# Kernel optimization log

Hardware: AMD Instinct MI355X
Metric: run time of the kernel (lower is better)

Reference implementation:

```python
import jax, jax.numpy as jnp
import numpy as np

N, E, F, G, C, L = 20000, 320000, 75, 64, 10, 5
EPS = 1e-5


def setup_inputs():
    key = jax.random.key(0)
    ks = jax.random.split(key, 16)
    x = jax.random.normal(ks[0], (N, 6), jnp.float32)
    edge_index = jax.random.randint(ks[1], (2, E), 0, N, dtype=jnp.int32)
    batch = jnp.sort(jax.random.randint(ks[2], (N,), 0, G, dtype=jnp.int32))
    gcn_w = jax.random.normal(ks[3], (6, F), jnp.float32) / np.sqrt(6.0)
    gcn_b = jnp.zeros((F,), jnp.float32)
    pre_w = jax.random.normal(ks[4], (L, 2 * F, F), jnp.float32) / np.sqrt(2.0 * F)
    pre_b = jnp.zeros((L, F), jnp.float32)
    post_w = jax.random.normal(ks[5], (L, 13 * F, F), jnp.float32) / np.sqrt(13.0 * F)
    post_b = jnp.zeros((L, F), jnp.float32)
    lin_w = jax.random.normal(ks[6], (L, F, F), jnp.float32) / np.sqrt(1.0 * F)
    lin_b = jnp.zeros((L, F), jnp.float32)
    bn_g = jnp.ones((L, F), jnp.float32)
    bn_b = jnp.zeros((L, F), jnp.float32)
    w1 = jax.random.normal(ks[7], (F, 50), jnp.float32) / np.sqrt(1.0 * F)
    b1 = jnp.zeros((50,), jnp.float32)
    w2 = jax.random.normal(ks[8], (50, 25), jnp.float32) / np.sqrt(50.0)
    b2 = jnp.zeros((25,), jnp.float32)
    w3 = jax.random.normal(ks[9], (25, C), jnp.float32) / np.sqrt(25.0)
    b3 = jnp.zeros((C,), jnp.float32)
    return dict(x=x, edge_index=edge_index, batch=batch, gcn_w=gcn_w, gcn_b=gcn_b,
                pre_w=pre_w, pre_b=pre_b, post_w=post_w, post_b=post_b,
                lin_w=lin_w, lin_b=lin_b, bn_g=bn_g, bn_b=bn_b,
                w1=w1, b1=b1, w2=w2, b2=b2, w3=w3, b3=b3)


def reference(x, edge_index, batch, gcn_w, gcn_b, pre_w, pre_b, post_w, post_b,
              lin_w, lin_b, bn_g, bn_b, w1, b1, w2, b2, w3, b3):
    row, col = edge_index[0], edge_index[1]  # messages flow row (j) -> col (i)
    ones_e = jnp.ones((E,), jnp.float32)

    # ---- GCNConv(6, 75) with self-loops and symmetric normalization ----
    xw = x @ gcn_w                                   # [N, F]
    deg = jax.ops.segment_sum(ones_e, col, N) + 1.0  # in-degree + self-loop
    dinv = 1.0 / jnp.sqrt(deg)
    norm_e = (dinv[row] * dinv[col])[:, None]        # [E, 1]
    h = jax.ops.segment_sum(norm_e * xw[row], col, N) + (dinv * dinv)[:, None] * xw + gcn_b

    # ---- degree-based scalers (shared by all PNA layers) ----
    cnt = jax.ops.segment_sum(ones_e, col, N)        # in-degree per node
    avg_log = jnp.mean(jnp.log(cnt + 1.0))           # avg_deg['log'] from this graph's degree histogram
    d = jnp.maximum(cnt, 1.0)
    amp = (jnp.log(d + 1.0) / avg_log)[:, None]      # amplification
    att = (avg_log / jnp.log(d + 1.0))[:, None]      # attenuation
    cnt_c = jnp.maximum(cnt, 1.0)[:, None]
    has_nb = (cnt > 0)[:, None]

    for l in range(L):
        # pre-MLP on [x_i, x_j] per edge
        m = jnp.concatenate([h[col], h[row]], axis=-1) @ pre_w[l] + pre_b[l]  # [E, F]
        s = jax.ops.segment_sum(m, col, N)
        mean = s / cnt_c
        mean_sq = jax.ops.segment_sum(m * m, col, N) / cnt_c
        std = jnp.sqrt(jax.nn.relu(mean_sq - mean * mean) + EPS)
        mn = jnp.where(has_nb, jax.ops.segment_min(m, col, N), 0.0)
        mx = jnp.where(has_nb, jax.ops.segment_max(m, col, N), 0.0)
        agg = jnp.concatenate([mean, mn, mx, std], axis=-1)          # [N, 4F]
        scaled = jnp.concatenate([agg, agg * amp, agg * att], -1)    # [N, 12F]
        o = jnp.concatenate([h, scaled], axis=-1) @ post_w[l] + post_b[l]  # post-MLP
        o = o @ lin_w[l] + lin_b[l]                                  # final lin
        mu = o.mean(axis=0)
        var = o.var(axis=0)
        o = (o - mu) / jnp.sqrt(var + EPS) * bn_g[l] + bn_b[l]       # BatchNorm (batch stats)
        h = jax.nn.relu(o)

    # ---- global_add_pool + MLP (dropout = identity in eval) ----
    g = jax.ops.segment_sum(h, batch, G)
    g = jax.nn.relu(g @ w1 + b1)
    g = jax.nn.relu(g @ w2 + b2)
    return g @ w3 + b3  # [G, C]
```

## Files before the change

### kernel.cpp

```cpp
#include <hip/hip_runtime.h>
#include <hip/hip_bf16.h>

#define NN 20000
#define EE 320000
#define FF 75
#define GG 64
#define LL 5
#define EPS 1e-5f

#define KUV 96
#define NUV 160
#define KPOST 384
#define NPOST 240
#define KLIN 96

typedef short bf16x8 __attribute__((ext_vector_type(8)));
typedef float f32x4 __attribute__((ext_vector_type(4)));

__device__ inline void gAtomicAdd(float* p, float v) { unsafeAtomicAdd(p, v); }

__device__ inline ushort f2bs(float x) {
    __hip_bfloat16 b = __float2bfloat16(x);
    return *(ushort*)&b;
}

__device__ inline float bs2f(ushort u) {
    unsigned int x = ((unsigned int)u) << 16;
    return __uint_as_float(x);
}


__global__ void count_kernel(const int* __restrict__ col, int* __restrict__ cnt, int E) {
    int e = blockIdx.x * blockDim.x + threadIdx.x;
    if (e < E) atomicAdd(&cnt[col[e]], 1);
}

__global__ void partial_kernel(const int* __restrict__ cnt, int* __restrict__ bsum, int N) {
    __shared__ int sh[256];
    int tid = threadIdx.x;
    int i = blockIdx.x * 256 + tid;
    sh[tid] = (i < N) ? cnt[i] : 0;
    __syncthreads();
    for (int s = 128; s > 0; s >>= 1) {
        if (tid < s) sh[tid] += sh[tid + s];
        __syncthreads();
    }
    if (tid == 0) bsum[blockIdx.x] = sh[0];
}

__global__ void scanb_kernel(const int* __restrict__ bsum, int* __restrict__ bbase,
                             int* __restrict__ offs, int NB) {
    __shared__ int sh[128];
    int tid = threadIdx.x;
    int v = (tid < NB) ? bsum[tid] : 0;
    sh[tid] = v;
    __syncthreads();
    for (int d = 1; d < 128; d <<= 1) {
        int t = (tid >= d) ? sh[tid - d] : 0;
        __syncthreads();
        sh[tid] += t;
        __syncthreads();
    }
    if (tid < NB) bbase[tid] = sh[tid] - v;
    if (tid == 0) offs[NN] = EE;
}

__global__ void offs_kernel(const int* __restrict__ cnt, const int* __restrict__ bbase,
                            int* __restrict__ offs, int* __restrict__ cursor, int N) {
    __shared__ int sh[256];
    int tid = threadIdx.x;
    int i = blockIdx.x * 256 + tid;
    int v = (i < N) ? cnt[i] : 0;
    sh[tid] = v;
    __syncthreads();
    for (int d = 1; d < 256; d <<= 1) {
        int t = (tid >= d) ? sh[tid - d] : 0;
        __syncthreads();
        sh[tid] += t;
        __syncthreads();
    }
    int excl = sh[tid] - v + bbase[blockIdx.x];
    if (i < N) { offs[i] = excl; cursor[i] = excl; }
}

__global__ void fill_kernel(const int* __restrict__ row, const int* __restrict__ col,
                            int* __restrict__ cursor, int* __restrict__ csr, int E) {
    int e = blockIdx.x * blockDim.x + threadIdx.x;
    if (e < E) {
        int c = col[e];
        int pos = atomicAdd(&cursor[c], 1);
        csr[pos] = row[e];
    }
}


__global__ void dinv_kernel(const int* __restrict__ cnt, float* __restrict__ dinv,
                            float* __restrict__ scal, int N) {
    __shared__ float red[256];
    int i = blockIdx.x * 256 + threadIdx.x;
    float lg = 0.f;
    if (i < N) {
        float c = (float)cnt[i];
        dinv[i] = 1.f / sqrtf(c + 1.f);
        lg = logf(c + 1.f);
    }
    red[threadIdx.x] = lg;
    __syncthreads();
    for (int s = 128; s > 0; s >>= 1) {
        if (threadIdx.x < s) red[threadIdx.x] += red[threadIdx.x + s];
        __syncthreads();
    }
    if (threadIdx.x == 0) gAtomicAdd(&scal[0], red[0]);
}


__global__ void xs_kernel(const float* __restrict__ x, const float* __restrict__ gw,
                          const float* __restrict__ dinv, ushort* __restrict__ xs, int N) {
    int idx = blockIdx.x * 256 + threadIdx.x;
    if (idx >= N * 80) return;
    int n = idx / 80, t = idx % 80;
    float v = 0.f;
    if (t < FF) {
        float acc = 0.f;
#pragma unroll
        for (int k = 0; k < 6; k++) acc += x[n * 6 + k] * gw[k * FF + t];
        v = dinv[n] * acc;
    }
    xs[idx] = f2bs(v);
}

__global__ __launch_bounds__(64) void gcn_kernel(
    const ushort* __restrict__ xs, const float* __restrict__ dinv,
    const int* __restrict__ offs, const int* __restrict__ csr,
    const float* __restrict__ gcn_b, const int* __restrict__ cnt,
    const float* __restrict__ scal, float* __restrict__ o2,
    float* __restrict__ amp, float* __restrict__ att, int N) {
    int i = blockIdx.x;
    int lane = threadIdx.x;
    int s0 = offs[i], s1 = offs[i + 1];
    if (lane < 40) {
        float a0 = 0.f, a1 = 0.f;
        int k = s0;
        for (; k + 1 < s1; k += 2) {
            int r0 = csr[k], r1 = csr[k + 1];
            ushort2 v0 = *(const ushort2*)(xs + (size_t)r0 * 80 + 2 * lane);
            ushort2 v1 = *(const ushort2*)(xs + (size_t)r1 * 80 + 2 * lane);
            a0 += bs2f(v0.x) + bs2f(v1.x);
            a1 += bs2f(v0.y) + bs2f(v1.y);
        }
        if (k < s1) {
            int r0 = csr[k];
            ushort2 v0 = *(const ushort2*)(xs + (size_t)r0 * 80 + 2 * lane);
            a0 += bs2f(v0.x);
            a1 += bs2f(v0.y);
        }
        ushort2 vs = *(const ushort2*)(xs + (size_t)i * 80 + 2 * lane);
        a0 += bs2f(vs.x);
        a1 += bs2f(vs.y);
        float di = dinv[i];
        int t0 = 2 * lane, t1 = 2 * lane + 1;
        if (t0 < FF) o2[(size_t)i * 80 + t0] = di * a0 + gcn_b[t0];
        if (t1 < FF) o2[(size_t)i * 80 + t1] = di * a1 + gcn_b[t1];
    } else if (lane == 63) {
        float al = scal[0] / (float)N;
        float d = fmaxf((float)cnt[i], 1.f);
        float lg = logf(d + 1.f);
        amp[i] = lg / al;
        att[i] = al / lg;
    }
}


#define S_UV (LL * NUV * KUV)
#define S_POST (LL * NPOST * KPOST)
#define S_LIN (LL * 80 * KLIN)

__global__ void prep_bt_kernel(const float* __restrict__ pre_w, const float* __restrict__ pre_b,
                               const float* __restrict__ post_w, const float* __restrict__ lin_w,
                               ushort* __restrict__ BTuv, ushort* __restrict__ BTpost,
                               ushort* __restrict__ BTlin) {
    int idx = blockIdx.x * 256 + threadIdx.x;
    if (idx < S_UV) {
        int l = idx / (NUV * KUV);
        int r = idx % (NUV * KUV);
        int c = r / KUV, k = r % KUV;
        float v = 0.f;
        if (k < FF) {
            if (c < FF) v = pre_w[((size_t)l * 150 + k) * FF + c];
            else if (c >= 80 && c < 80 + FF) v = pre_w[((size_t)l * 150 + FF + k) * FF + (c - 80)];
        } else if (k == FF && c < FF) {
            v = pre_b[l * FF + c];
        }
        BTuv[idx] = f2bs(v);
    } else if (idx < S_UV + S_POST) {
        int j = idx - S_UV;
        int l = j / (NPOST * KPOST);
        int r = j % (NPOST * KPOST);
        int c = r / KPOST, k = r % KPOST;
        float v = 0.f;
        if (k < FF) {
            if (c < FF) v = post_w[((size_t)l * 975 + k) * FF + c];
        } else if (k < 375) {
            if (c < FF) v = post_w[((size_t)l * 975 + k) * FF + c];
            else if (c >= 80 && c < 80 + FF) v = post_w[((size_t)l * 975 + k + 300) * FF + (c - 80)];
            else if (c >= 160 && c < 160 + FF) v = post_w[((size_t)l * 975 + k + 600) * FF + (c - 160)];
        }
        BTpost[j] = f2bs(v);
    } else if (idx < S_UV + S_POST + S_LIN) {
        int j = idx - S_UV - S_POST;
        int l = j / (80 * KLIN);
        int r = j % (80 * KLIN);
        int c = r / KLIN, k = r % KLIN;
        float v = (c < FF && k < FF) ? lin_w[((size_t)l * FF + k) * FF + c] : 0.f;
        BTlin[j] = f2bs(v);
    }
}


__global__ __launch_bounds__(64) void uv_bn_kernel(
    const float* __restrict__ o2, const float* __restrict__ slots,
    const float* __restrict__ bg, const float* __restrict__ bb, int apply_bn,
    const ushort* __restrict__ BT, float* __restrict__ U, ushort* __restrict__ Vb,
    ushort* __restrict__ hagg) {
    __shared__ float ssL[160];
    int lane = threadIdx.x;
    int col16 = lane & 15, quad = lane >> 4;
    int n = blockIdx.x * 16 + col16;
    const float* orow = o2 + (size_t)n * 80;
    const ushort* bbase = BT + (size_t)col16 * KUV + quad * 8;

    if (apply_bn) {
        for (int c = lane; c < 80; c += 64) {
            if (c < FF) {
                float su = 0.f, sq = 0.f;
#pragma unroll 8
                for (int s = 0; s < 32; s++) {
                    su += slots[s * 160 + c];
                    sq += slots[s * 160 + 80 + c];
                }
                float mu = su * (1.f / (float)NN);
                float var = sq * (1.f / (float)NN) - mu * mu;
                float sc = bg[c] * rsqrtf(var + EPS);
                ssL[c] = sc;
                ssL[80 + c] = bb[c] - mu * sc;
            } else {
                ssL[c] = 0.f;
                ssL[80 + c] = 0.f;
            }
        }
        __syncthreads();
    }

    f32x4 acc[10];
#pragma unroll
    for (int i = 0; i < 10; i++) acc[i] = (f32x4){0.f, 0.f, 0.f, 0.f};

#pragma unroll
    for (int kt = 0; kt < 3; kt++) {
        int kb = kt * 32 + quad * 8;
        bf16x8 af;
        if (kb < 80) {
            float4 v0 = *(const float4*)(orow + kb);
            float4 v1 = *(const float4*)(orow + kb + 4);
            float vv[8] = {v0.x, v0.y, v0.z, v0.w, v1.x, v1.y, v1.z, v1.w};
#pragma unroll
            for (int j = 0; j < 8; j++) {
                int k = kb + j;
                float v = vv[j];
                if (apply_bn) v = fmaxf(v * ssL[k] + ssL[80 + k], 0.f);
                ushort b = (k < FF) ? f2bs(v) : (k == FF ? (ushort)0x3F80 : (ushort)0);
                af[j] = (short)b;
            }
            if (kb < FF) {
                *(bf16x8*)(hagg + (size_t)n * KPOST + kb) = af;
            }
        } else {
            af = (bf16x8){0, 0, 0, 0, 0, 0, 0, 0};
        }
#pragma unroll
        for (int nt = 0; nt < 10; nt++) {
            bf16x8 bfr = *(const bf16x8*)(bbase + nt * (16 * KUV) + kt * 32);
            acc[nt] = __builtin_amdgcn_mfma_f32_16x16x32_bf16(af, bfr, acc[nt], 0, 0, 0);
        }
    }
    int n0 = blockIdx.x * 16;
#pragma unroll
    for (int nt = 0; nt < 10; nt++) {
        int col = nt * 16 + col16;
#pragma unroll
        for (int r = 0; r < 4; r++) {
            int nn = n0 + quad * 4 + r;
            if (col < FF) U[(size_t)nn * 80 + col] = acc[nt][r];
            else if (col >= 80 && col < 80 + FF) Vb[(size_t)nn * 80 + (col - 80)] = f2bs(acc[nt][r]);
        }
    }
}


__global__ __launch_bounds__(64) void post_lin_kernel(
    const ushort* __restrict__ A, const ushort* __restrict__ BT,
    const ushort* __restrict__ BL, const float* __restrict__ amp,
    const float* __restrict__ att, float* __restrict__ o2,
    float* __restrict__ slots) {
    __shared__ __align__(16) ushort olds[16 * 104];
    int lane = threadIdx.x;
    int col16 = lane & 15, quad = lane >> 4;
    int n0 = blockIdx.x * 16;
    const ushort* arow = A + (size_t)(n0 + col16) * KPOST + quad * 8;
    const ushort* bbase = BT + (size_t)col16 * KPOST + quad * 8;

    f32x4 acc[15];
#pragma unroll
    for (int i = 0; i < 15; i++) acc[i] = (f32x4){0.f, 0.f, 0.f, 0.f};

#pragma unroll 2
    for (int kt = 0; kt < 12; kt++) {
        bf16x8 af = *(const bf16x8*)(arow + kt * 32);
#pragma unroll
        for (int nt = 0; nt < 15; nt++) {
            bf16x8 bfr = *(const bf16x8*)(bbase + nt * (16 * KPOST) + kt * 32);
            acc[nt] = __builtin_amdgcn_mfma_f32_16x16x32_bf16(af, bfr, acc[nt], 0, 0, 0);
        }
    }
    float ampv[4], attv[4];
#pragma unroll
    for (int r = 0; r < 4; r++) {
        int n = n0 + quad * 4 + r;
        ampv[r] = amp[n];
        attv[r] = att[n];
    }
#pragma unroll
    for (int g = 0; g < 5; g++) {
        int col = g * 16 + col16;
#pragma unroll
        for (int r = 0; r < 4; r++) {
            float ov = acc[g][r] + ampv[r] * acc[g + 5][r] + attv[r] * acc[g + 10][r];
            olds[(quad * 4 + r) * 104 + col] = (col < FF) ? f2bs(ov) : (ushort)0;
        }
    }
    *(ushort4*)(olds + (lane >> 2) * 104 + 80 + (lane & 3) * 4) = (ushort4){0, 0, 0, 0};
    __syncthreads();

    f32x4 acc2[5];
#pragma unroll
    for (int i = 0; i < 5; i++) acc2[i] = (f32x4){0.f, 0.f, 0.f, 0.f};
    const ushort* blbase = BL + (size_t)col16 * KLIN + quad * 8;
#pragma unroll
    for (int kt = 0; kt < 3; kt++) {
        bf16x8 af = *(const bf16x8*)(olds + col16 * 104 + kt * 32 + quad * 8);
#pragma unroll
        for (int nt = 0; nt < 5; nt++) {
            bf16x8 bfr = *(const bf16x8*)(blbase + nt * (16 * KLIN) + kt * 32);
            acc2[nt] = __builtin_amdgcn_mfma_f32_16x16x32_bf16(af, bfr, acc2[nt], 0, 0, 0);
        }
    }
    float* slot = slots + (blockIdx.x & 31) * 160;
#pragma unroll
    for (int nt = 0; nt < 5; nt++) {
        int col = nt * 16 + col16;
        float s = 0.f, q = 0.f;
#pragma unroll
        for (int r = 0; r < 4; r++) {
            int n = n0 + quad * 4 + r;
            float v = acc2[nt][r];
            if (col < FF) {
                o2[(size_t)n * 80 + col] = v;
                s += v;
                q += v * v;
            }
        }
        s += __shfl_xor(s, 16); s += __shfl_xor(s, 32);
        q += __shfl_xor(q, 16); q += __shfl_xor(q, 32);
        if (lane < 16 && col < FF) {
            gAtomicAdd(&slot[col], s);
            gAtomicAdd(&slot[80 + col], q);
        }
    }
}


__global__ __launch_bounds__(64) void edge_agg_kernel(
    const float* __restrict__ U, const ushort* __restrict__ V,
    const int* __restrict__ offs, const int* __restrict__ csr,
    const int* __restrict__ cnt, ushort* __restrict__ hagg) {
    int i = blockIdx.x;
    int lane = threadIdx.x;
    int s0 = offs[i], s1 = offs[i + 1];
    if (lane < 40) {
        float2 uiv = *(const float2*)(U + (size_t)i * 80 + 2 * lane);
        float ui0 = uiv.x, ui1 = uiv.y;
        float sa0 = 0.f, sq0 = 0.f, mn0 = 1e30f, mx0 = -1e30f;
        float sa1 = 0.f, sq1 = 0.f, mn1 = 1e30f, mx1 = -1e30f;
        int k = s0;
        for (; k + 1 < s1; k += 2) {
            int r0 = csr[k], r1 = csr[k + 1];
            ushort2 v0 = *(const ushort2*)(V + (size_t)r0 * 80 + 2 * lane);
            ushort2 v1 = *(const ushort2*)(V + (size_t)r1 * 80 + 2 * lane);
            float a0 = ui0 + bs2f(v0.x), b0 = ui0 + bs2f(v1.x);
            float a1 = ui1 + bs2f(v0.y), b1 = ui1 + bs2f(v1.y);
            sa0 += a0 + b0; sq0 += a0 * a0 + b0 * b0;
            mn0 = fminf(mn0, fminf(a0, b0)); mx0 = fmaxf(mx0, fmaxf(a0, b0));
            sa1 += a1 + b1; sq1 += a1 * a1 + b1 * b1;
            mn1 = fminf(mn1, fminf(a1, b1)); mx1 = fmaxf(mx1, fmaxf(a1, b1));
        }
        if (k < s1) {
            int r0 = csr[k];
            ushort2 v0 = *(const ushort2*)(V + (size_t)r0 * 80 + 2 * lane);
            float a0 = ui0 + bs2f(v0.x);
            float a1 = ui1 + bs2f(v0.y);
            sa0 += a0; sq0 += a0 * a0; mn0 = fminf(mn0, a0); mx0 = fmaxf(mx0, a0);
            sa1 += a1; sq1 += a1 * a1; mn1 = fminf(mn1, a1); mx1 = fmaxf(mx1, a1);
        }
        int c = cnt[i];
        float cc = fmaxf((float)c, 1.f);
        ushort* a = hagg + (size_t)i * KPOST + FF;
        int t0 = 2 * lane, t1 = 2 * lane + 1;
        {
            float mean = sa0 / cc;
            float stdv = sqrtf(fmaxf(sq0 / cc - mean * mean, 0.f) + EPS);
            if (c == 0) { mn0 = 0.f; mx0 = 0.f; }
            if (t0 < FF) {
                a[t0] = f2bs(mean);
                a[FF + t0] = f2bs(mn0);
                a[2 * FF + t0] = f2bs(mx0);
                a[3 * FF + t0] = f2bs(stdv);
            }
        }
        {
            float mean = sa1 / cc;
            float stdv = sqrtf(fmaxf(sq1 / cc - mean * mean, 0.f) + EPS);
            if (c == 0) { mn1 = 0.f; mx1 = 0.f; }
            if (t1 < FF) {
                a[t1] = f2bs(mean);
                a[FF + t1] = f2bs(mn1);
                a[2 * FF + t1] = f2bs(mx1);
                a[3 * FF + t1] = f2bs(stdv);
            }
        }
    } else if (lane >= 48 && lane < 57) {
        hagg[(size_t)i * KPOST + 375 + (lane - 48)] = 0;
    }
}


__global__ void pool_kernel(const float* __restrict__ o2, const float* __restrict__ slots,
                            const float* __restrict__ bg, const float* __restrict__ bb,
                            const int* __restrict__ batch, float* __restrict__ g, int N) {
    __shared__ float acc[GG * FF];
    __shared__ float ssL[160];
    int tid = threadIdx.x;
    int n0 = blockIdx.x * 64;
    int n1 = min(n0 + 64, N);
    if (n0 >= N) return;
    for (int c = tid; c < 80; c += 256) {
        if (c < FF) {
            float su = 0.f, sq = 0.f;
#pragma unroll 8
            for (int s = 0; s < 32; s++) {
                su += slots[s * 160 + c];
                sq += slots[s * 160 + 80 + c];
            }
            float mu = su * (1.f / (float)NN);
            float var = sq * (1.f / (float)NN) - mu * mu;
            float sc = bg[c] * rsqrtf(var + EPS);
            ssL[c] = sc;
            ssL[80 + c] = bb[c] - mu * sc;
        } else {
            ssL[c] = 0.f;
            ssL[80 + c] = 0.f;
        }
    }
    int g0 = batch[n0];
    int g1 = batch[n1 - 1];
    int range = g1 - g0 + 1;
    for (int i = tid; i < range * FF; i += 256) acc[i] = 0.f;
    __syncthreads();
    int rows = n1 - n0;
    for (int idx = tid; idx < rows * FF; idx += 256) {
        int r = idx / FF, c = idx % FF;
        int n = n0 + r;
        float val = fmaxf(o2[(size_t)n * 80 + c] * ssL[c] + ssL[80 + c], 0.f);
        gAtomicAdd(&acc[(batch[n] - g0) * FF + c], val);
    }
    __syncthreads();
    for (int i = tid; i < range * FF; i += 256) gAtomicAdd(&g[g0 * FF + i], acc[i]);
}

__global__ void mlp_kernel(const float* __restrict__ g,
                           const float* __restrict__ w1, const float* __restrict__ b1,
                           const float* __restrict__ w2, const float* __restrict__ b2,
                           const float* __restrict__ w3, const float* __restrict__ b3,
                           float* __restrict__ out) {
    __shared__ float gr[FF], h1[50], h2[25];
    int gi = blockIdx.x, t = threadIdx.x;
    for (int j = t; j < FF; j += 64) gr[j] = g[gi * FF + j];
    __syncthreads();
    if (t < 50) {
        float a = b1[t];
        for (int k = 0; k < FF; k++) a += gr[k] * w1[k * 50 + t];
        h1[t] = fmaxf(a, 0.f);
    }
    __syncthreads();
    if (t < 25) {
        float a = b2[t];
        for (int k = 0; k < 50; k++) a += h1[k] * w2[k * 25 + t];
        h2[t] = fmaxf(a, 0.f);
    }
    __syncthreads();
    if (t < 10) {
        float a = b3[t];
        for (int k = 0; k < 25; k++) a += h2[k] * w3[k * 10 + t];
        out[gi * 10 + t] = a;
    }
}


extern "C" void kernel_launch(void* const* d_in, const int* in_sizes, int n_in,
                              void* d_out, int out_size, void* d_ws, size_t ws_size,
                              hipStream_t stream) {
    const float* x = (const float*)d_in[0];
    const int* ei = (const int*)d_in[1];
    const int* batch = (const int*)d_in[2];
    const float* gcn_w = (const float*)d_in[3];
    const float* gcn_b = (const float*)d_in[4];
    const float* pre_w = (const float*)d_in[5];
    const float* pre_b = (const float*)d_in[6];
    const float* post_w = (const float*)d_in[7];
    const float* lin_w = (const float*)d_in[9];
    const float* bn_g = (const float*)d_in[11];
    const float* bn_b = (const float*)d_in[12];
    const float* w1 = (const float*)d_in[13];
    const float* b1 = (const float*)d_in[14];
    const float* w2 = (const float*)d_in[15];
    const float* b2 = (const float*)d_in[16];
    const float* w3 = (const float*)d_in[17];
    const float* b3 = (const float*)d_in[18];
    float* out = (float*)d_out;

    const int* row = ei;
    const int* col = ei + EE;

    char* ws = (char*)d_ws;
    size_t off = 0;
    auto alloc = [&](size_t bytes) {
        char* p = ws + off;
        off += (bytes + 255) & ~(size_t)255;
        return p;
    };
    int* cnt = (int*)alloc(NN * 4);
    int* offs = (int*)alloc((NN + 1) * 4);
    int* cursor = (int*)alloc(NN * 4);
    int* csr = (int*)alloc(EE * 4);
    int* bsum = (int*)alloc(128 * 4);
    int* bbase = (int*)alloc(128 * 4);
    float* dinv = (float*)alloc(NN * 4);
    float* amp = (float*)alloc(NN * 4);
    float* att = (float*)alloc(NN * 4);
    float* scal = (float*)alloc((1 + LL * 32 * 160) * 4);
    float* slotbase = scal + 1;
    float* o2 = (float*)alloc((size_t)NN * 80 * 4);
    float* ubuf = (float*)alloc((size_t)NN * 80 * 4);
    ushort* vbuf = (ushort*)alloc((size_t)NN * 80 * 2);
    ushort* hagg = (ushort*)alloc((size_t)NN * KPOST * 2);
    ushort* BTuv = (ushort*)alloc((size_t)S_UV * 2);
    ushort* BTpost = (ushort*)alloc((size_t)S_POST * 2);
    ushort* BTlin = (ushort*)alloc((size_t)S_LIN * 2);
    float* gbuf = (float*)alloc(GG * FF * 4);

    hipMemsetAsync(cnt, 0, NN * 4, stream);
    hipMemsetAsync(scal, 0, (1 + LL * 32 * 160) * 4, stream);
    hipMemsetAsync(gbuf, 0, GG * FF * 4, stream);

    const int B = 256;
    const int NB = (NN + 255) / 256;
    count_kernel<<<(EE + B - 1) / B, B, 0, stream>>>(col, cnt, EE);
    dinv_kernel<<<NB, B, 0, stream>>>(cnt, dinv, scal, NN);
    partial_kernel<<<NB, B, 0, stream>>>(cnt, bsum, NN);
    scanb_kernel<<<1, 128, 0, stream>>>(bsum, bbase, offs, NB);
    offs_kernel<<<NB, B, 0, stream>>>(cnt, bbase, offs, cursor, NN);
    fill_kernel<<<(EE + B - 1) / B, B, 0, stream>>>(row, col, cursor, csr, EE);
    xs_kernel<<<(NN * 80 + B - 1) / B, B, 0, stream>>>(x, gcn_w, dinv, vbuf, NN);
    gcn_kernel<<<NN, 64, 0, stream>>>(vbuf, dinv, offs, csr, gcn_b, cnt, scal,
                                      o2, amp, att, NN);
    {
        int tot = S_UV + S_POST + S_LIN;
        prep_bt_kernel<<<(tot + B - 1) / B, B, 0, stream>>>(pre_w, pre_b, post_w, lin_w,
                                                            BTuv, BTpost, BTlin);
    }

    const int GS = NN / 16;
    for (int l = 0; l < LL; l++) {
        float* slots_prev = slotbase + (l - 1) * 32 * 160;
        float* slots = slotbase + l * 32 * 160;
        int lp = (l > 0) ? (l - 1) : 0;

        uv_bn_kernel<<<GS, 64, 0, stream>>>(o2, (l == 0) ? slotbase : slots_prev,
                                            bn_g + lp * FF, bn_b + lp * FF, (l > 0) ? 1 : 0,
                                            BTuv + (size_t)l * NUV * KUV, ubuf, vbuf, hagg);
        edge_agg_kernel<<<NN, 64, 0, stream>>>(ubuf, vbuf, offs, csr, cnt, hagg);
        post_lin_kernel<<<GS, 64, 0, stream>>>(hagg, BTpost + (size_t)l * NPOST * KPOST,
                                               BTlin + (size_t)l * 80 * KLIN, amp, att,
                                               o2, slots);
    }

    pool_kernel<<<(NN + 63) / 64, 256, 0, stream>>>(o2, slotbase + (LL - 1) * 32 * 160,
                                                    bn_g + (LL - 1) * FF, bn_b + (LL - 1) * FF,
                                                    batch, gbuf, NN);
    mlp_kernel<<<GG, 64, 0, stream>>>(gbuf, w1, b1, w2, b2, w3, b3, out);
}
```

Baseline: 509.8 us.

## Fuse edge aggregation into post/lin GEMM kernel via shared-memory staging

Merges the per-node edge aggregation kernel into the post-MLP/final-linear kernel. Each 256-thread block builds its 16-row aggregated bf16 input tile in LDS (recomputing the BN+ReLU'd h from o2) instead of writing and rereading a global hagg buffer. The GEMM N-tiles are split across four waves, with wave 0 taking a fifth tile. Separately, the dinv and partial-sum setup kernels are merged into one launch. This removes a large global round trip and per-layer launches, but aggregation now runs with only 16 nodes per block, which may cut latency hiding for the gather, and wave 0 does extra work.

```diff
diff --git a/kernel.cpp b/kernel.cpp
--- a/kernel.cpp
+++ b/kernel.cpp
@@ -13,6 +13,7 @@
 #define KPOST 384
 #define NPOST 240
 #define KLIN 96
+#define ASTR 392
 
 typedef short bf16x8 __attribute__((ext_vector_type(8)));
 typedef float f32x4 __attribute__((ext_vector_type(4)));
@@ -35,17 +36,31 @@
     if (e < E) atomicAdd(&cnt[col[e]], 1);
 }
 
-__global__ void partial_kernel(const int* __restrict__ cnt, int* __restrict__ bsum, int N) {
-    __shared__ int sh[256];
+__global__ void dinv_partial_kernel(const int* __restrict__ cnt, float* __restrict__ dinv,
+                                    float* __restrict__ scal, int* __restrict__ bsum, int N) {
+    __shared__ float red[256];
+    __shared__ int redi[256];
     int tid = threadIdx.x;
     int i = blockIdx.x * 256 + tid;
-    sh[tid] = (i < N) ? cnt[i] : 0;
+    float lg = 0.f;
+    int cv = 0;
+    if (i < N) {
+        cv = cnt[i];
+        float c = (float)cv;
+        dinv[i] = 1.f / sqrtf(c + 1.f);
+        lg = logf(c + 1.f);
+    }
+    red[tid] = lg;
+    redi[tid] = cv;
     __syncthreads();
     for (int s = 128; s > 0; s >>= 1) {
-        if (tid < s) sh[tid] += sh[tid + s];
+        if (tid < s) { red[tid] += red[tid + s]; redi[tid] += redi[tid + s]; }
         __syncthreads();
     }
-    if (tid == 0) bsum[blockIdx.x] = sh[0];
+    if (tid == 0) {
+        gAtomicAdd(&scal[0], red[0]);
+        bsum[blockIdx.x] = redi[0];
+    }
 }
 
 __global__ void scanb_kernel(const int* __restrict__ bsum, int* __restrict__ bbase,
@@ -91,26 +106,6 @@
         int pos = atomicAdd(&cursor[c], 1);
         csr[pos] = row[e];
     }
-}
-
-
-__global__ void dinv_kernel(const int* __restrict__ cnt, float* __restrict__ dinv,
-                            float* __restrict__ scal, int N) {
-    __shared__ float red[256];
-    int i = blockIdx.x * 256 + threadIdx.x;
-    float lg = 0.f;
-    if (i < N) {
-        float c = (float)cnt[i];
-        dinv[i] = 1.f / sqrtf(c + 1.f);
-        lg = logf(c + 1.f);
-    }
-    red[threadIdx.x] = lg;
-    __syncthreads();
-    for (int s = 128; s > 0; s >>= 1) {
-        if (threadIdx.x < s) red[threadIdx.x] += red[threadIdx.x + s];
-        __syncthreads();
-    }
-    if (threadIdx.x == 0) gAtomicAdd(&scal[0], red[0]);
 }
 
 
@@ -220,8 +215,7 @@
 __global__ __launch_bounds__(64) void uv_bn_kernel(
     const float* __restrict__ o2, const float* __restrict__ slots,
     const float* __restrict__ bg, const float* __restrict__ bb, int apply_bn,
-    const ushort* __restrict__ BT, float* __restrict__ U, ushort* __restrict__ Vb,
-    ushort* __restrict__ hagg) {
+    const ushort* __restrict__ BT, float* __restrict__ U, ushort* __restrict__ Vb) {
     __shared__ float ssL[160];
     int lane = threadIdx.x;
     int col16 = lane & 15, quad = lane >> 4;
@@ -271,9 +265,6 @@
                 ushort b = (k < FF) ? f2bs(v) : (k == FF ? (ushort)0x3F80 : (ushort)0);
                 af[j] = (short)b;
             }
-            if (kb < FF) {
-                *(bf16x8*)(hagg + (size_t)n * KPOST + kb) = af;
-            }
         } else {
             af = (bf16x8){0, 0, 0, 0, 0, 0, 0, 0};
         }
@@ -297,29 +288,130 @@
 }
 
 
-__global__ __launch_bounds__(64) void post_lin_kernel(
-    const ushort* __restrict__ A, const ushort* __restrict__ BT,
-    const ushort* __restrict__ BL, const float* __restrict__ amp,
-    const float* __restrict__ att, float* __restrict__ o2,
+__global__ __launch_bounds__(256) void agg_post_lin_kernel(
+    const float* __restrict__ o2io, const float* __restrict__ slots_prev,
+    const float* __restrict__ bg, const float* __restrict__ bb, int apply_bn,
+    const float* __restrict__ U, const ushort* __restrict__ V,
+    const int* __restrict__ offs, const int* __restrict__ csr, const int* __restrict__ cnt,
+    const ushort* __restrict__ BT, const ushort* __restrict__ BL,
+    const float* __restrict__ amp, const float* __restrict__ att,
     float* __restrict__ slots) {
+    __shared__ float ssL[160];
+    __shared__ __align__(16) ushort aggL[16 * ASTR];
     __shared__ __align__(16) ushort olds[16 * 104];
-    int lane = threadIdx.x;
-    int col16 = lane & 15, quad = lane >> 4;
+    int tid = threadIdx.x, w = tid >> 6, lane = tid & 63;
+    int col16 = lane & 15, quad = lane >> 4, kseg = quad * 8;
     int n0 = blockIdx.x * 16;
-    const ushort* arow = A + (size_t)(n0 + col16) * KPOST + quad * 8;
-    const ushort* bbase = BT + (size_t)col16 * KPOST + quad * 8;
-
-    f32x4 acc[15];
-#pragma unroll
-    for (int i = 0; i < 15; i++) acc[i] = (f32x4){0.f, 0.f, 0.f, 0.f};
-
+
+    if (apply_bn) {
+        for (int c = tid; c < 80; c += 256) {
+            if (c < FF) {
+                float su = 0.f, sq = 0.f;
+#pragma unroll 8
+                for (int s = 0; s < 32; s++) {
+                    su += slots_prev[s * 160 + c];
+                    sq += slots_prev[s * 160 + 80 + c];
+                }
+                float mu = su * (1.f / (float)NN);
+                float var = sq * (1.f / (float)NN) - mu * mu;
+                float sc = bg[c] * rsqrtf(var + EPS);
+                ssL[c] = sc;
+                ssL[80 + c] = bb[c] - mu * sc;
+            }
+        }
+        __syncthreads();
+    }
+
+    for (int idx = tid; idx < 16 * 80; idx += 256) {
+        int r = idx / 80, c = idx % 80;
+        if (c < FF) {
+            float v = o2io[(size_t)(n0 + r) * 80 + c];
+            if (apply_bn) v = fmaxf(v * ssL[c] + ssL[80 + c], 0.f);
+            aggL[r * ASTR + c] = f2bs(v);
+        }
+    }
+    for (int idx = tid; idx < 16 * 9; idx += 256) {
+        int r = idx / 9, c = 375 + idx % 9;
+        aggL[r * ASTR + c] = 0;
+    }
+
+    for (int rr = 0; rr < 4; rr++) {
+        int r = w * 4 + rr;
+        int i = n0 + r;
+        if (lane < 40) {
+            int s0 = offs[i], s1 = offs[i + 1];
+            float2 uiv = *(const float2*)(U + (size_t)i * 80 + 2 * lane);
+            float ui0 = uiv.x, ui1 = uiv.y;
+            float sa0 = 0.f, sq0 = 0.f, mn0 = 1e30f, mx0 = -1e30f;
+            float sa1 = 0.f, sq1 = 0.f, mn1 = 1e30f, mx1 = -1e30f;
+            int k = s0;
+            for (; k + 1 < s1; k += 2) {
+                int r0 = csr[k], r1 = csr[k + 1];
+                ushort2 v0 = *(const ushort2*)(V + (size_t)r0 * 80 + 2 * lane);
+                ushort2 v1 = *(const ushort2*)(V + (size_t)r1 * 80 + 2 * lane);
+                float a0 = ui0 + bs2f(v0.x), b0 = ui0 + bs2f(v1.x);
+                float a1 = ui1 + bs2f(v0.y), b1 = ui1 + bs2f(v1.y);
+                sa0 += a0 + b0; sq0 += a0 * a0 + b0 * b0;
+                mn0 = fminf(mn0, fminf(a0, b0)); mx0 = fmaxf(mx0, fmaxf(a0, b0));
+                sa1 += a1 + b1; sq1 += a1 * a1 + b1 * b1;
+                mn1 = fminf(mn1, fminf(a1, b1)); mx1 = fmaxf(mx1, fmaxf(a1, b1));
+            }
+            if (k < s1) {
+                int r0 = csr[k];
+                ushort2 v0 = *(const ushort2*)(V + (size_t)r0 * 80 + 2 * lane);
+                float a0 = ui0 + bs2f(v0.x);
+                float a1 = ui1 + bs2f(v0.y);
+                sa0 += a0; sq0 += a0 * a0; mn0 = fminf(mn0, a0); mx0 = fmaxf(mx0, a0);
+                sa1 += a1; sq1 += a1 * a1; mn1 = fminf(mn1, a1); mx1 = fmaxf(mx1, a1);
+            }
+            int c = cnt[i];
+            float cc = fmaxf((float)c, 1.f);
+            ushort* a = aggL + r * ASTR;
+            int t0 = 2 * lane, t1 = 2 * lane + 1;
+            {
+                float mean = sa0 / cc;
+                float stdv = sqrtf(fmaxf(sq0 / cc - mean * mean, 0.f) + EPS);
+                if (c == 0) { mn0 = 0.f; mx0 = 0.f; }
+                if (t0 < FF) {
+                    a[75 + t0] = f2bs(mean);
+                    a[150 + t0] = f2bs(mn0);
+                    a[225 + t0] = f2bs(mx0);
+                    a[300 + t0] = f2bs(stdv);
+                }
+            }
+            {
+                float mean = sa1 / cc;
+                float stdv = sqrtf(fmaxf(sq1 / cc - mean * mean, 0.f) + EPS);
+                if (c == 0) { mn1 = 0.f; mx1 = 0.f; }
+                if (t1 < FF) {
+                    a[75 + t1] = f2bs(mean);
+                    a[150 + t1] = f2bs(mn1);
+                    a[225 + t1] = f2bs(mx1);
+                    a[300 + t1] = f2bs(stdv);
+                }
+            }
+        }
+    }
+    __syncthreads();
+
+    bool two_tri = (w == 0);
+    f32x4 acc[6];
+#pragma unroll
+    for (int i = 0; i < 6; i++) acc[i] = (f32x4){0.f, 0.f, 0.f, 0.f};
 #pragma unroll 2
     for (int kt = 0; kt < 12; kt++) {
-        bf16x8 af = *(const bf16x8*)(arow + kt * 32);
-#pragma unroll
-        for (int nt = 0; nt < 15; nt++) {
-            bf16x8 bfr = *(const bf16x8*)(bbase + nt * (16 * KPOST) + kt * 32);
-            acc[nt] = __builtin_amdgcn_mfma_f32_16x16x32_bf16(af, bfr, acc[nt], 0, 0, 0);
+        bf16x8 af = *(const bf16x8*)(aggL + col16 * ASTR + kt * 32 + kseg);
+#pragma unroll
+        for (int j = 0; j < 3; j++) {
+            bf16x8 bfr = *(const bf16x8*)(BT + (size_t)((w + 5 * j) * 16 + col16) * KPOST + kt * 32 + kseg);
+            acc[j] = __builtin_amdgcn_mfma_f32_16x16x32_bf16(af, bfr, acc[j], 0, 0, 0);
+        }
+        if (two_tri) {
+#pragma unroll
+            for (int j = 0; j < 3; j++) {
+                bf16x8 bfr = *(const bf16x8*)(BT + (size_t)((4 + 5 * j) * 16 + col16) * KPOST + kt * 32 + kseg);
+                acc[3 + j] = __builtin_amdgcn_mfma_f32_16x16x32_bf16(af, bfr, acc[3 + j], 0, 0, 0);
+            }
         }
     }
     float ampv[4], attv[4];
@@ -329,42 +421,54 @@
         ampv[r] = amp[n];
         attv[r] = att[n];
     }
-#pragma unroll
-    for (int g = 0; g < 5; g++) {
-        int col = g * 16 + col16;
+    {
+        int col = w * 16 + col16;
 #pragma unroll
         for (int r = 0; r < 4; r++) {
-            float ov = acc[g][r] + ampv[r] * acc[g + 5][r] + attv[r] * acc[g + 10][r];
+            float ov = acc[0][r] + ampv[r] * acc[1][r] + attv[r] * acc[2][r];
             olds[(quad * 4 + r) * 104 + col] = (col < FF) ? f2bs(ov) : (ushort)0;
         }
     }
-    *(ushort4*)(olds + (lane >> 2) * 104 + 80 + (lane & 3) * 4) = (ushort4){0, 0, 0, 0};
-    __syncthreads();
-
-    f32x4 acc2[5];
-#pragma unroll
-    for (int i = 0; i < 5; i++) acc2[i] = (f32x4){0.f, 0.f, 0.f, 0.f};
-    const ushort* blbase = BL + (size_t)col16 * KLIN + quad * 8;
+    if (two_tri) {
+        int col = 64 + col16;
+#pragma unroll
+        for (int r = 0; r < 4; r++) {
+            float ov = acc[3][r] + ampv[r] * acc[4][r] + attv[r] * acc[5][r];
+            olds[(quad * 4 + r) * 104 + col] = (col < FF) ? f2bs(ov) : (ushort)0;
+        }
+    }
+    if (w == 1) {
+        *(ushort4*)(olds + (lane >> 2) * 104 + 80 + (lane & 3) * 4) = (ushort4){0, 0, 0, 0};
+    }
+    __syncthreads();
+
+    f32x4 acc2[2];
+    acc2[0] = (f32x4){0.f, 0.f, 0.f, 0.f};
+    acc2[1] = (f32x4){0.f, 0.f, 0.f, 0.f};
 #pragma unroll
     for (int kt = 0; kt < 3; kt++) {
-        bf16x8 af = *(const bf16x8*)(olds + col16 * 104 + kt * 32 + quad * 8);
-#pragma unroll
-        for (int nt = 0; nt < 5; nt++) {
-            bf16x8 bfr = *(const bf16x8*)(blbase + nt * (16 * KLIN) + kt * 32);
-            acc2[nt] = __builtin_amdgcn_mfma_f32_16x16x32_bf16(af, bfr, acc2[nt], 0, 0, 0);
+        bf16x8 af = *(const bf16x8*)(olds + col16 * 104 + kt * 32 + kseg);
+        bf16x8 b0 = *(const bf16x8*)(BL + (size_t)(w * 16 + col16) * KLIN + kt * 32 + kseg);
+        acc2[0] = __builtin_amdgcn_mfma_f32_16x16x32_bf16(af, b0, acc2[0], 0, 0, 0);
+        if (two_tri) {
+            bf16x8 b1 = *(const bf16x8*)(BL + (size_t)(64 + col16) * KLIN + kt * 32 + kseg);
+            acc2[1] = __builtin_amdgcn_mfma_f32_16x16x32_bf16(af, b1, acc2[1], 0, 0, 0);
         }
     }
     float* slot = slots + (blockIdx.x & 31) * 160;
-#pragma unroll
-    for (int nt = 0; nt < 5; nt++) {
+    float* o2w = (float*)o2io;
+#pragma unroll
+    for (int ti = 0; ti < 2; ti++) {
+        if (ti == 1 && !two_tri) break;
+        int nt = (ti == 0) ? w : 4;
         int col = nt * 16 + col16;
         float s = 0.f, q = 0.f;
 #pragma unroll
         for (int r = 0; r < 4; r++) {
             int n = n0 + quad * 4 + r;
-            float v = acc2[nt][r];
+            float v = acc2[ti][r];
             if (col < FF) {
-                o2[(size_t)n * 80 + col] = v;
+                o2w[(size_t)n * 80 + col] = v;
                 s += v;
                 q += v * v;
             }
@@ -375,70 +479,6 @@
             gAtomicAdd(&slot[col], s);
             gAtomicAdd(&slot[80 + col], q);
         }
-    }
-}
-
-
-__global__ __launch_bounds__(64) void edge_agg_kernel(
-    const float* __restrict__ U, const ushort* __restrict__ V,
-    const int* __restrict__ offs, const int* __restrict__ csr,
-    const int* __restrict__ cnt, ushort* __restrict__ hagg) {
-    int i = blockIdx.x;
-    int lane = threadIdx.x;
-    int s0 = offs[i], s1 = offs[i + 1];
-    if (lane < 40) {
-        float2 uiv = *(const float2*)(U + (size_t)i * 80 + 2 * lane);
-        float ui0 = uiv.x, ui1 = uiv.y;
-        float sa0 = 0.f, sq0 = 0.f, mn0 = 1e30f, mx0 = -1e30f;
-        float sa1 = 0.f, sq1 = 0.f, mn1 = 1e30f, mx1 = -1e30f;
-        int k = s0;
-        for (; k + 1 < s1; k += 2) {
-            int r0 = csr[k], r1 = csr[k + 1];
-            ushort2 v0 = *(const ushort2*)(V + (size_t)r0 * 80 + 2 * lane);
-            ushort2 v1 = *(const ushort2*)(V + (size_t)r1 * 80 + 2 * lane);
-            float a0 = ui0 + bs2f(v0.x), b0 = ui0 + bs2f(v1.x);
-            float a1 = ui1 + bs2f(v0.y), b1 = ui1 + bs2f(v1.y);
-            sa0 += a0 + b0; sq0 += a0 * a0 + b0 * b0;
-            mn0 = fminf(mn0, fminf(a0, b0)); mx0 = fmaxf(mx0, fmaxf(a0, b0));
-            sa1 += a1 + b1; sq1 += a1 * a1 + b1 * b1;
-            mn1 = fminf(mn1, fminf(a1, b1)); mx1 = fmaxf(mx1, fmaxf(a1, b1));
-        }
-        if (k < s1) {
-            int r0 = csr[k];
-            ushort2 v0 = *(const ushort2*)(V + (size_t)r0 * 80 + 2 * lane);
-            float a0 = ui0 + bs2f(v0.x);
-            float a1 = ui1 + bs2f(v0.y);
-            sa0 += a0; sq0 += a0 * a0; mn0 = fminf(mn0, a0); mx0 = fmaxf(mx0, a0);
-            sa1 += a1; sq1 += a1 * a1; mn1 = fminf(mn1, a1); mx1 = fmaxf(mx1, a1);
-        }
-        int c = cnt[i];
-        float cc = fmaxf((float)c, 1.f);
-        ushort* a = hagg + (size_t)i * KPOST + FF;
-        int t0 = 2 * lane, t1 = 2 * lane + 1;
-        {
-            float mean = sa0 / cc;
-            float stdv = sqrtf(fmaxf(sq0 / cc - mean * mean, 0.f) + EPS);
-            if (c == 0) { mn0 = 0.f; mx0 = 0.f; }
-            if (t0 < FF) {
-                a[t0] = f2bs(mean);
-                a[FF + t0] = f2bs(mn0);
-                a[2 * FF + t0] = f2bs(mx0);
-                a[3 * FF + t0] = f2bs(stdv);
-            }
-        }
-        {
-            float mean = sa1 / cc;
-            float stdv = sqrtf(fmaxf(sq1 / cc - mean * mean, 0.f) + EPS);
-            if (c == 0) { mn1 = 0.f; mx1 = 0.f; }
-            if (t1 < FF) {
-                a[t1] = f2bs(mean);
-                a[FF + t1] = f2bs(mn1);
-                a[2 * FF + t1] = f2bs(mx1);
-                a[3 * FF + t1] = f2bs(stdv);
-            }
-        }
-    } else if (lane >= 48 && lane < 57) {
-        hagg[(size_t)i * KPOST + 375 + (lane - 48)] = 0;
     }
 }
 
@@ -561,7 +601,6 @@
     float* o2 = (float*)alloc((size_t)NN * 80 * 4);
     float* ubuf = (float*)alloc((size_t)NN * 80 * 4);
     ushort* vbuf = (ushort*)alloc((size_t)NN * 80 * 2);
-    ushort* hagg = (ushort*)alloc((size_t)NN * KPOST * 2);
     ushort* BTuv = (ushort*)alloc((size_t)S_UV * 2);
     ushort* BTpost = (ushort*)alloc((size_t)S_POST * 2);
     ushort* BTlin = (ushort*)alloc((size_t)S_LIN * 2);
@@ -574,8 +613,7 @@
     const int B = 256;
     const int NB = (NN + 255) / 256;
     count_kernel<<<(EE + B - 1) / B, B, 0, stream>>>(col, cnt, EE);
-    dinv_kernel<<<NB, B, 0, stream>>>(cnt, dinv, scal, NN);
-    partial_kernel<<<NB, B, 0, stream>>>(cnt, bsum, NN);
+    dinv_partial_kernel<<<NB, B, 0, stream>>>(cnt, dinv, scal, bsum, NN);
     scanb_kernel<<<1, 128, 0, stream>>>(bsum, bbase, offs, NB);
     offs_kernel<<<NB, B, 0, stream>>>(cnt, bbase, offs, cursor, NN);
     fill_kernel<<<(EE + B - 1) / B, B, 0, stream>>>(row, col, cursor, csr, EE);
@@ -593,14 +631,15 @@
         float* slots_prev = slotbase + (l - 1) * 32 * 160;
         float* slots = slotbase + l * 32 * 160;
         int lp = (l > 0) ? (l - 1) : 0;
-
-        uv_bn_kernel<<<GS, 64, 0, stream>>>(o2, (l == 0) ? slotbase : slots_prev,
-                                            bn_g + lp * FF, bn_b + lp * FF, (l > 0) ? 1 : 0,
-                                            BTuv + (size_t)l * NUV * KUV, ubuf, vbuf, hagg);
-        edge_agg_kernel<<<NN, 64, 0, stream>>>(ubuf, vbuf, offs, csr, cnt, hagg);
-        post_lin_kernel<<<GS, 64, 0, stream>>>(hagg, BTpost + (size_t)l * NPOST * KPOST,
-                                               BTlin + (size_t)l * 80 * KLIN, amp, att,
-                                               o2, slots);
+        int ab = (l > 0) ? 1 : 0;
+        const float* sp = (l == 0) ? slotbase : slots_prev;
+
+        uv_bn_kernel<<<GS, 64, 0, stream>>>(o2, sp, bn_g + lp * FF, bn_b + lp * FF, ab,
+                                            BTuv + (size_t)l * NUV * KUV, ubuf, vbuf);
+        agg_post_lin_kernel<<<GS, 256, 0, stream>>>(
+            o2, sp, bn_g + lp * FF, bn_b + lp * FF, ab, ubuf, vbuf, offs, csr, cnt,
+            BTpost + (size_t)l * NPOST * KPOST, BTlin + (size_t)l * 80 * KLIN,
+            amp, att, slots);
     }
 
     pool_kernel<<<(NN + 63) / 64, 256, 0, stream>>>(o2, slotbase + (LL - 1) * 32 * 160,
```

Measured after the change: 536.2 us. 5.2% more time.
